# Kernel tuning notes

Hardware: AMD Instinct MI355X
Metric: run time of the kernel (lower is better)

The kernel has to match this reference:

```python
import jax, jax.numpy as jnp
import numpy as np

NUM_EXPERTS = 8
TOP_K = 2


def setup_inputs() -> dict:
    key = jax.random.key(0)
    k1, k2, k3, k4, k5 = jax.random.split(key, 5)
    B, S, H, F, E = 4, 1024, 1024, 2048, NUM_EXPERTS
    return {
        "hidden_states": jax.random.normal(k1, (B, S, H), dtype=jnp.float32),
        "gate_w": jax.random.normal(k2, (H, E), dtype=jnp.float32) * 0.02,
        "w1": jax.random.normal(k3, (E, H, F), dtype=jnp.float32) * 0.02,
        "w2": jax.random.normal(k4, (E, F, H), dtype=jnp.float32) * 0.02,
        "w3": jax.random.normal(k5, (E, H, F), dtype=jnp.float32) * 0.02,
    }


def reference(hidden_states, gate_w, w1, w2, w3):
    """Mixtral MoE block: router softmax -> top-2 -> SwiGLU expert FFN -> weighted combine.

    Same math as Gmm (sort + grouped GEMM + scatter): each token passes through its
    top-k experts' FFNs (silu(x@w1) * (x@w3)) @ w2, then the outputs are combined
    with the renormalized top-k routing weights.
    """
    B, S, H = hidden_states.shape
    E = w1.shape[0]
    x = hidden_states.reshape(-1, H)                       # [m, H]
    m = x.shape[0]

    router_logits = x @ gate_w                             # [m, E]
    probs = jax.nn.softmax(router_logits, axis=-1)
    top_w, top_i = jax.lax.top_k(probs, TOP_K)             # [m, k]
    top_w = top_w / jnp.sum(top_w, axis=-1, keepdims=True)

    # dense routing matrix [m, E] (top-k indices are distinct per row)
    route = jnp.zeros((m, E), dtype=x.dtype)
    route = route.at[jnp.arange(m)[:, None], top_i].set(top_w)

    out = jnp.zeros_like(x)
    for e in range(E):  # fixed small expert count; accumulate to keep memory low
        h = jax.nn.silu(x @ w1[e]) * (x @ w3[e])           # [m, F]
        out = out + route[:, e:e + 1] * (h @ w2[e])        # [m, H]

    return out.reshape(B, S, H)
```

## Files before the change

### kernel.cpp

```cpp
#include <hip/hip_runtime.h>

typedef __attribute__((ext_vector_type(8))) short bf16x8;
typedef __attribute__((ext_vector_type(4))) float f32x4;

#define MTOK 4096
#define HD 1024
#define FD 2048
#define NEXP 8
#define MAXT 72

struct Ctl {
  int counts[NEXP];
  int cursor[NEXP];
  int totalTiles;
  int _pad[7];
  int4 tileMap[MAXT];
  int topE[MTOK][2];
  float topW[MTOK][2];
  int pos[MTOK][2];
  int rowTok[2 * MTOK];
};

__device__ __forceinline__ unsigned short f2bf(float f) {
  unsigned int u = __float_as_uint(f);
  unsigned int r = u + 0x7fffu + ((u >> 16) & 1u);
  return (unsigned short)(r >> 16);
}
__device__ __forceinline__ float bf2f(unsigned short s) {
  return __uint_as_float(((unsigned int)s) << 16);
}
__device__ __forceinline__ unsigned int pk2(float a, float b) {
  return (unsigned int)f2bf(a) | ((unsigned int)f2bf(b) << 16);
}
__device__ __forceinline__ void gload16(const void* g, void* l) {
  __builtin_amdgcn_global_load_lds(
      (const __attribute__((address_space(1))) void*)g,
      (__attribute__((address_space(3))) void*)l, 16, 0, 0);
}

__global__ void k_tr(const float* __restrict__ in, unsigned short* __restrict__ outp,
                     int K, int N) {
  __shared__ float tile[64][65];
  int ntn = N >> 6, ntk = K >> 6;
  int bid = blockIdx.x;
  int e = bid / (ntk * ntn);
  int rem = bid % (ntk * ntn);
  int kt = rem / ntn, nt = rem % ntn;
  const float* src = in + (size_t)e * K * N + (size_t)(kt * 64) * N + nt * 64;
  unsigned short* dst = outp + (size_t)e * N * K + (size_t)(nt * 64) * K + kt * 64;
  int t = threadIdx.x;
  int nl = t & 63, kq = t >> 6;
#pragma unroll
  for (int i = 0; i < 16; i++) {
    int kl = kq * 16 + i;
    tile[kl][nl] = src[(size_t)kl * N + nl];
  }
  __syncthreads();
  int n2 = t >> 2, kc = (t & 3) * 16;
  unsigned int pk[8];
#pragma unroll
  for (int j = 0; j < 8; j++)
    pk[j] = pk2(tile[kc + 2 * j][n2], tile[kc + 2 * j + 1][n2]);
  *(uint4*)(dst + (size_t)n2 * K + kc) = make_uint4(pk[0], pk[1], pk[2], pk[3]);
  *(uint4*)(dst + (size_t)n2 * K + kc + 8) = make_uint4(pk[4], pk[5], pk[6], pk[7]);
}

__global__ void k_cvt_x(const float* __restrict__ x, unsigned short* __restrict__ xb) {
  int i = blockIdx.x * 256 + threadIdx.x;
  const float4* s = (const float4*)x;
  float4 a = s[i * 2], b = s[i * 2 + 1];
  *(uint4*)(xb + (size_t)i * 8) =
      make_uint4(pk2(a.x, a.y), pk2(a.z, a.w), pk2(b.x, b.y), pk2(b.z, b.w));
}

__global__ void k_router(const float* __restrict__ x, const float* __restrict__ gw,
                         Ctl* __restrict__ ctl) {
  int gt = blockIdx.x * 256 + threadIdx.x;
  int tok = gt >> 6;
  int lane = gt & 63;
  const float* xr = x + (size_t)tok * HD;
  float acc[NEXP] = {};
#pragma unroll
  for (int it = 0; it < 4; it++) {
    int h0 = it * 256 + lane * 4;
    float4 xv = *(const float4*)(xr + h0);
    float xs[4] = {xv.x, xv.y, xv.z, xv.w};
#pragma unroll
    for (int j = 0; j < 4; j++) {
      float4 g0 = *(const float4*)(gw + (size_t)(h0 + j) * 8);
      float4 g1 = *(const float4*)(gw + (size_t)(h0 + j) * 8 + 4);
      acc[0] += xs[j] * g0.x; acc[1] += xs[j] * g0.y;
      acc[2] += xs[j] * g0.z; acc[3] += xs[j] * g0.w;
      acc[4] += xs[j] * g1.x; acc[5] += xs[j] * g1.y;
      acc[6] += xs[j] * g1.z; acc[7] += xs[j] * g1.w;
    }
  }
#pragma unroll
  for (int off = 32; off > 0; off >>= 1) {
#pragma unroll
    for (int e = 0; e < NEXP; e++) acc[e] += __shfl_xor(acc[e], off);
  }
  if (lane == 0) {
    float l0 = -1e30f, l1 = -1e30f; int i0 = 0, i1 = 0;
#pragma unroll
    for (int e = 0; e < NEXP; e++) {
      float v = acc[e];
      if (v > l0) { l1 = l0; i1 = i0; l0 = v; i0 = e; }
      else if (v > l1) { l1 = v; i1 = e; }
    }
    float w0 = 1.f / (1.f + __expf(l1 - l0));
    ctl->topE[tok][0] = i0; ctl->topE[tok][1] = i1;
    ctl->topW[tok][0] = w0; ctl->topW[tok][1] = 1.f - w0;
  }
}

__global__ void k_count(Ctl* __restrict__ ctl) {
  __shared__ int lcnt[NEXP];
  int t = threadIdx.x;
  if (t < NEXP) lcnt[t] = 0;
  __syncthreads();
  int tok = blockIdx.x * 512 + t;
  atomicAdd(&lcnt[ctl->topE[tok][0]], 1);
  atomicAdd(&lcnt[ctl->topE[tok][1]], 1);
  __syncthreads();
  if (t < NEXP && lcnt[t]) atomicAdd(&ctl->counts[t], lcnt[t]);
}

__global__ void k_setup(Ctl* __restrict__ ctl) {
  if (threadIdx.x == 0 && blockIdx.x == 0) {
    int off = 0, t = 0;
    for (int e = 0; e < NEXP; e++) {
      ctl->cursor[e] = off;
      int c = ctl->counts[e];
      int nt = (c + 127) >> 7;
      for (int i = 0; i < nt; i++) {
        if (t < MAXT)
          ctl->tileMap[t] = make_int4(e, off + i * 128, min(128, c - i * 128), 0);
        t++;
      }
      off += c;
    }
    ctl->totalTiles = t;
    for (; t < MAXT; t++) ctl->tileMap[t] = make_int4(0, 0, 0, 0);
  }
}

__global__ void k_scatter(Ctl* __restrict__ ctl) {
  __shared__ int lcur[NEXP];
  __shared__ int gbase[NEXP];
  int t = threadIdx.x;
  int tok = blockIdx.x * 512 + t;
  if (t < NEXP) lcur[t] = 0;
  __syncthreads();
  int e0 = ctl->topE[tok][0];
  int e1 = ctl->topE[tok][1];
  int r0 = atomicAdd(&lcur[e0], 1);
  int r1 = atomicAdd(&lcur[e1], 1);
  __syncthreads();
  if (t < NEXP) gbase[t] = lcur[t] ? atomicAdd(&ctl->cursor[t], lcur[t]) : 0;
  __syncthreads();
  int p0 = gbase[e0] + r0;
  int p1 = gbase[e1] + r1;
  ctl->rowTok[p0] = tok; ctl->pos[tok][0] = p0;
  ctl->rowTok[p1] = tok; ctl->pos[tok][1] = p1;
}

__launch_bounds__(512, 2)
__global__ void k_gemm1(const unsigned short* __restrict__ xb,
                        const unsigned short* __restrict__ w1t,
                        const unsigned short* __restrict__ w3t,
                        unsigned short* __restrict__ hg,
                        const Ctl* __restrict__ ctl) {
  __shared__ __align__(1024) unsigned char lds[2][3][8192];
  int nwg = MAXT * (FD / 128);
  int bid = blockIdx.x;
  int swz = (bid & 7) * (nwg >> 3) + (bid >> 3);
  int rt = swz % MAXT, ct = swz / MAXT;
  int4 tm = ctl->tileMap[rt];
  if (tm.z == 0) return;
  int e = tm.x, grow0 = tm.y, nrows = tm.z;
  int t = threadIdx.x;

  int r = t >> 2;
  int cl = (t & 3) ^ ((r >> 1) & 3);
  int rA = min(r, nrows - 1);
  int tok = ctl->rowTok[grow0 + rA];
  const unsigned short* aG  = xb  + (size_t)tok * HD + cl * 8;
  const unsigned short* b1G = w1t + ((size_t)e * FD + ct * 128 + r) * HD + cl * 8;
  const unsigned short* b3G = w3t + ((size_t)e * FD + ct * 128 + r) * HD + cl * 8;
  unsigned char* ldsDstA  = &lds[0][0][t * 16];
  unsigned char* ldsDstB1 = &lds[0][1][t * 16];
  unsigned char* ldsDstB3 = &lds[0][2][t * 16];

  int lane = t & 63, wv = t >> 6, wr = wv >> 2, wc = wv & 3;
  int lm = lane & 15, lk = lane >> 4;
  int aOff[4], bOff[2];
#pragma unroll
  for (int ma = 0; ma < 4; ma++) {
    int row = wr * 64 + ma * 16 + lm;
    aOff[ma] = row * 64 + ((lk ^ ((row >> 1) & 3)) << 4);
  }
#pragma unroll
  for (int nb = 0; nb < 2; nb++) {
    int row = wc * 32 + nb * 16 + lm;
    bOff[nb] = row * 64 + ((lk ^ ((row >> 1) & 3)) << 4);
  }

  f32x4 accA[4][2] = {};
  f32x4 accC[4][2] = {};

  const int NK = HD / 32;
  gload16(aG, ldsDstA); gload16(b1G, ldsDstB1); gload16(b3G, ldsDstB3);
  for (int kt = 0; kt < NK; kt++) {
    int b = kt & 1;
    if (kt + 1 < NK) {
      size_t ko = (size_t)(kt + 1) * 32;
      int nbuf = b ^ 1;
      gload16(aG + ko,  ldsDstA  + nbuf * 3 * 8192);
      gload16(b1G + ko, ldsDstB1 + nbuf * 3 * 8192);
      gload16(b3G + ko, ldsDstB3 + nbuf * 3 * 8192);
      asm volatile("s_waitcnt vmcnt(3)" ::: "memory");
    } else {
      asm volatile("s_waitcnt vmcnt(0)" ::: "memory");
    }
    __builtin_amdgcn_s_barrier();
    asm volatile("" ::: "memory");
    const unsigned char* pA  = &lds[b][0][0];
    const unsigned char* pB1 = &lds[b][1][0];
    const unsigned char* pB3 = &lds[b][2][0];
    bf16x8 af[4], bf1[2], bf3[2];
#pragma unroll
    for (int ma = 0; ma < 4; ma++) af[ma] = *(const bf16x8*)(pA + aOff[ma]);
#pragma unroll
    for (int nb = 0; nb < 2; nb++) {
      bf1[nb] = *(const bf16x8*)(pB1 + bOff[nb]);
      bf3[nb] = *(const bf16x8*)(pB3 + bOff[nb]);
    }
#pragma unroll
    for (int nb = 0; nb < 2; nb++)
#pragma unroll
      for (int ma = 0; ma < 4; ma++) {
        accA[ma][nb] = __builtin_amdgcn_mfma_f32_16x16x32_bf16(af[ma], bf1[nb], accA[ma][nb], 0, 0, 0);
        accC[ma][nb] = __builtin_amdgcn_mfma_f32_16x16x32_bf16(af[ma], bf3[nb], accC[ma][nb], 0, 0, 0);
      }
    asm volatile("" ::: "memory");
    __builtin_amdgcn_s_barrier();
  }

#pragma unroll
  for (int ma = 0; ma < 4; ma++) {
    int lrowBase = wr * 64 + ma * 16 + lk * 4;
#pragma unroll
    for (int nb = 0; nb < 2; nb++) {
      int col = ct * 128 + wc * 32 + nb * 16 + lm;
#pragma unroll
      for (int rr = 0; rr < 4; rr++) {
        int lrow = lrowBase + rr;
        if (lrow < nrows) {
          float a = accA[ma][nb][rr];
          float c = accC[ma][nb][rr];
          float hv = a / (1.f + __expf(-a)) * c;
          hg[(size_t)(grow0 + lrow) * FD + col] = f2bf(hv);
        }
      }
    }
  }
}

__launch_bounds__(512, 2)
__global__ void k_gemm2(const unsigned short* __restrict__ hg,
                        const unsigned short* __restrict__ w2t,
                        unsigned short* __restrict__ og,
                        const Ctl* __restrict__ ctl) {
  __shared__ __align__(1024) unsigned char lds[2][2][8192];
  int nwg = MAXT * (HD / 128);
  int bid = blockIdx.x;
  int swz = (bid & 7) * (nwg >> 3) + (bid >> 3);
  int rt = swz % MAXT, ct = swz / MAXT;
  int4 tm = ctl->tileMap[rt];
  if (tm.z == 0) return;
  int e = tm.x, grow0 = tm.y, nrows = tm.z;
  int t = threadIdx.x;

  int r = t >> 2;
  int cl = (t & 3) ^ ((r >> 1) & 3);
  int rA = min(r, nrows - 1);
  const unsigned short* aG = hg  + (size_t)(grow0 + rA) * FD + cl * 8;
  const unsigned short* bG = w2t + ((size_t)e * HD + ct * 128 + r) * FD + cl * 8;
  unsigned char* ldsDstA = &lds[0][0][t * 16];
  unsigned char* ldsDstB = &lds[0][1][t * 16];

  int lane = t & 63, wv = t >> 6, wr = wv >> 2, wc = wv & 3;
  int lm = lane & 15, lk = lane >> 4;
  int aOff[4], bOff[2];
#pragma unroll
  for (int ma = 0; ma < 4; ma++) {
    int row = wr * 64 + ma * 16 + lm;
    aOff[ma] = row * 64 + ((lk ^ ((row >> 1) & 3)) << 4);
  }
#pragma unroll
  for (int nb = 0; nb < 2; nb++) {
    int row = wc * 32 + nb * 16 + lm;
    bOff[nb] = row * 64 + ((lk ^ ((row >> 1) & 3)) << 4);
  }

  f32x4 acc[4][2] = {};
  const int NK = FD / 32;
  gload16(aG, ldsDstA); gload16(bG, ldsDstB);
  for (int kt = 0; kt < NK; kt++) {
    int b = kt & 1;
    if (kt + 1 < NK) {
      size_t ko = (size_t)(kt + 1) * 32;
      int nbuf = b ^ 1;
      gload16(aG + ko, ldsDstA + nbuf * 2 * 8192);
      gload16(bG + ko, ldsDstB + nbuf * 2 * 8192);
      asm volatile("s_waitcnt vmcnt(2)" ::: "memory");
    } else {
      asm volatile("s_waitcnt vmcnt(0)" ::: "memory");
    }
    __builtin_amdgcn_s_barrier();
    asm volatile("" ::: "memory");
    const unsigned char* pA = &lds[b][0][0];
    const unsigned char* pB = &lds[b][1][0];
    bf16x8 af[4], bfr[2];
#pragma unroll
    for (int ma = 0; ma < 4; ma++) af[ma] = *(const bf16x8*)(pA + aOff[ma]);
#pragma unroll
    for (int nb = 0; nb < 2; nb++) bfr[nb] = *(const bf16x8*)(pB + bOff[nb]);
#pragma unroll
    for (int nb = 0; nb < 2; nb++)
#pragma unroll
      for (int ma = 0; ma < 4; ma++)
        acc[ma][nb] = __builtin_amdgcn_mfma_f32_16x16x32_bf16(af[ma], bfr[nb], acc[ma][nb], 0, 0, 0);
    asm volatile("" ::: "memory");
    __builtin_amdgcn_s_barrier();
  }

#pragma unroll
  for (int ma = 0; ma < 4; ma++) {
    int lrowBase = wr * 64 + ma * 16 + lk * 4;
#pragma unroll
    for (int nb = 0; nb < 2; nb++) {
      int col = ct * 128 + wc * 32 + nb * 16 + lm;
#pragma unroll
      for (int rr = 0; rr < 4; rr++) {
        int lrow = lrowBase + rr;
        if (lrow < nrows)
          og[(size_t)(grow0 + lrow) * HD + col] = f2bf(acc[ma][nb][rr]);
      }
    }
  }
}

__global__ void k_combine(const unsigned short* __restrict__ og, float* __restrict__ out,
                          const Ctl* __restrict__ ctl) {
  int tok = blockIdx.x;
  int tid = threadIdx.x;
  int p0 = ctl->pos[tok][0], p1 = ctl->pos[tok][1];
  float w0 = ctl->topW[tok][0], w1 = ctl->topW[tok][1];
  uint2 a = *(const uint2*)(og + (size_t)p0 * HD + tid * 4);
  uint2 b = *(const uint2*)(og + (size_t)p1 * HD + tid * 4);
  float4 o;
  o.x = w0 * bf2f((unsigned short)(a.x & 0xffffu)) + w1 * bf2f((unsigned short)(b.x & 0xffffu));
  o.y = w0 * bf2f((unsigned short)(a.x >> 16))     + w1 * bf2f((unsigned short)(b.x >> 16));
  o.z = w0 * bf2f((unsigned short)(a.y & 0xffffu)) + w1 * bf2f((unsigned short)(b.y & 0xffffu));
  o.w = w0 * bf2f((unsigned short)(a.y >> 16))     + w1 * bf2f((unsigned short)(b.y >> 16));
  *(float4*)(out + (size_t)tok * HD + tid * 4) = o;
}

extern "C" void kernel_launch(void* const* d_in, const int* in_sizes, int n_in,
                              void* d_out, int out_size, void* d_ws, size_t ws_size,
                              hipStream_t stream) {
  const float* x  = (const float*)d_in[0];
  const float* gw = (const float*)d_in[1];
  const float* w1 = (const float*)d_in[2];
  const float* w2 = (const float*)d_in[3];
  const float* w3 = (const float*)d_in[4];
  float* out = (float*)d_out;

  char* ws = (char*)d_ws;
  unsigned short* hg  = (unsigned short*)(ws);
  unsigned short* og  = (unsigned short*)(ws + (size_t)(32u << 20));
  unsigned short* xb  = (unsigned short*)(ws + (size_t)(48u << 20));
  unsigned short* wAt = (unsigned short*)(ws + (size_t)(56u << 20));
  unsigned short* wBt = (unsigned short*)(ws + (size_t)(88u << 20));
  Ctl* ctl = (Ctl*)(ws + (size_t)(120u << 20));

  hipMemsetAsync(ctl->counts, 0, sizeof(int) * NEXP, stream);
  k_tr<<<dim3(8 * 16 * 32), 256, 0, stream>>>(w1, wAt, HD, FD);
  k_tr<<<dim3(8 * 16 * 32), 256, 0, stream>>>(w3, wBt, HD, FD);
  k_cvt_x<<<dim3(2048), 256, 0, stream>>>(x, xb);
  k_router<<<dim3(MTOK / 4), 256, 0, stream>>>(x, gw, ctl);
  k_count<<<dim3(MTOK / 512), 512, 0, stream>>>(ctl);
  k_setup<<<1, 64, 0, stream>>>(ctl);
  k_scatter<<<dim3(MTOK / 512), 512, 0, stream>>>(ctl);
  k_gemm1<<<dim3(MAXT * (FD / 128)), 512, 0, stream>>>(xb, wAt, wBt, hg, ctl);
  k_tr<<<dim3(8 * 32 * 16), 256, 0, stream>>>(w2, wAt, FD, HD);
  k_gemm2<<<dim3(MAXT * (HD / 128)), 512, 0, stream>>>(hg, wAt, og, ctl);
  k_combine<<<dim3(MTOK), 256, 0, stream>>>(og, out, ctl);
}
```

Measured before the change: 400.6 us.

## Fuse prep kernels, vectorize transpose, parallelize setup, retile gemm2 to 128x64

Merges the w1/w3 transposes and the x conversion into one prep launch, and moves the counts memset into the router kernel. The transpose now does float4 loads into a padded tile. Tile-map setup is spread across 64 lanes instead of one thread. gemm2 moves from 512 threads with 128x128 tiles to 256 threads with 128x64 tiles, doubling the number of workgroups. This trades per-block B reuse for more parallelism, since gemm2 otherwise fills the GPU with few blocks.

```diff
diff --git a/kernel.cpp b/kernel.cpp
--- a/kernel.cpp
+++ b/kernel.cpp
@@ -38,22 +38,22 @@
       (__attribute__((address_space(3))) void*)l, 16, 0, 0);
 }
 
-__global__ void k_tr(const float* __restrict__ in, unsigned short* __restrict__ outp,
-                     int K, int N) {
-  __shared__ float tile[64][65];
+__device__ __forceinline__ void tr_body(const float* __restrict__ in,
+                                        unsigned short* __restrict__ outp,
+                                        int K, int N, int bid, float (*tile)[68]) {
   int ntn = N >> 6, ntk = K >> 6;
-  int bid = blockIdx.x;
   int e = bid / (ntk * ntn);
   int rem = bid % (ntk * ntn);
   int kt = rem / ntn, nt = rem % ntn;
   const float* src = in + (size_t)e * K * N + (size_t)(kt * 64) * N + nt * 64;
   unsigned short* dst = outp + (size_t)e * N * K + (size_t)(nt * 64) * K + kt * 64;
   int t = threadIdx.x;
-  int nl = t & 63, kq = t >> 6;
-#pragma unroll
-  for (int i = 0; i < 16; i++) {
-    int kl = kq * 16 + i;
-    tile[kl][nl] = src[(size_t)kl * N + nl];
+  int nl4 = t & 15, kr = t >> 4;
+#pragma unroll
+  for (int i = 0; i < 4; i++) {
+    int row = kr + i * 16;
+    float4 v = *(const float4*)(src + (size_t)row * N + nl4 * 4);
+    *(float4*)&tile[row][nl4 * 4] = v;
   }
   __syncthreads();
   int n2 = t >> 2, kc = (t & 3) * 16;
@@ -65,16 +65,34 @@
   *(uint4*)(dst + (size_t)n2 * K + kc + 8) = make_uint4(pk[4], pk[5], pk[6], pk[7]);
 }
 
-__global__ void k_cvt_x(const float* __restrict__ x, unsigned short* __restrict__ xb) {
-  int i = blockIdx.x * 256 + threadIdx.x;
-  const float4* s = (const float4*)x;
-  float4 a = s[i * 2], b = s[i * 2 + 1];
-  *(uint4*)(xb + (size_t)i * 8) =
-      make_uint4(pk2(a.x, a.y), pk2(a.z, a.w), pk2(b.x, b.y), pk2(b.z, b.w));
+__global__ void k_prep(const float* __restrict__ w1, const float* __restrict__ w3,
+                       const float* __restrict__ x,
+                       unsigned short* __restrict__ w1t, unsigned short* __restrict__ w3t,
+                       unsigned short* __restrict__ xb) {
+  __shared__ float tile[64][68];
+  int bid = blockIdx.x;
+  if (bid < 4096) {
+    tr_body(w1, w1t, HD, FD, bid, tile);
+  } else if (bid < 8192) {
+    tr_body(w3, w3t, HD, FD, bid - 4096, tile);
+  } else {
+    int i = (bid - 8192) * 256 + threadIdx.x;
+    const float4* s = (const float4*)x;
+    float4 a = s[i * 2], b = s[i * 2 + 1];
+    *(uint4*)(xb + (size_t)i * 8) =
+        make_uint4(pk2(a.x, a.y), pk2(a.z, a.w), pk2(b.x, b.y), pk2(b.z, b.w));
+  }
+}
+
+__global__ void k_tr(const float* __restrict__ in, unsigned short* __restrict__ outp,
+                     int K, int N) {
+  __shared__ float tile[64][68];
+  tr_body(in, outp, K, N, blockIdx.x, tile);
 }
 
 __global__ void k_router(const float* __restrict__ x, const float* __restrict__ gw,
                          Ctl* __restrict__ ctl) {
+  if (blockIdx.x == 0 && threadIdx.x < NEXP) ctl->counts[threadIdx.x] = 0;
   int gt = blockIdx.x * 256 + threadIdx.x;
   int tok = gt >> 6;
   int lane = gt & 63;
@@ -127,21 +145,27 @@
 }
 
 __global__ void k_setup(Ctl* __restrict__ ctl) {
-  if (threadIdx.x == 0 && blockIdx.x == 0) {
-    int off = 0, t = 0;
-    for (int e = 0; e < NEXP; e++) {
-      ctl->cursor[e] = off;
-      int c = ctl->counts[e];
-      int nt = (c + 127) >> 7;
-      for (int i = 0; i < nt; i++) {
-        if (t < MAXT)
-          ctl->tileMap[t] = make_int4(e, off + i * 128, min(128, c - i * 128), 0);
-        t++;
-      }
-      off += c;
-    }
-    ctl->totalTiles = t;
-    for (; t < MAXT; t++) ctl->tileMap[t] = make_int4(0, 0, 0, 0);
+  int lane = threadIdx.x;
+  int myC[NEXP], myOff[NEXP], myTb[NEXP];
+  int off = 0, t = 0;
+#pragma unroll
+  for (int e = 0; e < NEXP; e++) {
+    int c = ctl->counts[e];
+    myC[e] = c; myOff[e] = off; myTb[e] = t;
+    off += c; t += (c + 127) >> 7;
+  }
+  if (lane < NEXP) ctl->cursor[lane] = myOff[lane];
+  if (lane == 0) ctl->totalTiles = t;
+  for (int i = lane; i < MAXT; i += 64) {
+    int4 v = make_int4(0, 0, 0, 0);
+    if (i < t) {
+      int e = 0;
+#pragma unroll
+      for (int q = 1; q < NEXP; q++) if (myTb[q] <= i) e = q;
+      int j = i - myTb[e];
+      v = make_int4(e, myOff[e] + j * 128, min(128, myC[e] - j * 128), 0);
+    }
+    ctl->tileMap[i] = v;
   }
 }
 
@@ -267,13 +291,13 @@
   }
 }
 
-__launch_bounds__(512, 2)
+__launch_bounds__(256, 2)
 __global__ void k_gemm2(const unsigned short* __restrict__ hg,
                         const unsigned short* __restrict__ w2t,
                         unsigned short* __restrict__ og,
                         const Ctl* __restrict__ ctl) {
-  __shared__ __align__(1024) unsigned char lds[2][2][8192];
-  int nwg = MAXT * (HD / 128);
+  __shared__ __align__(1024) unsigned char lds[2][12288];
+  int nwg = MAXT * (HD / 64);
   int bid = blockIdx.x;
   int swz = (bid & 7) * (nwg >> 3) + (bid >> 3);
   int rt = swz % MAXT, ct = swz / MAXT;
@@ -282,15 +306,19 @@
   int e = tm.x, grow0 = tm.y, nrows = tm.z;
   int t = threadIdx.x;
 
-  int r = t >> 2;
-  int cl = (t & 3) ^ ((r >> 1) & 3);
-  int rA = min(r, nrows - 1);
-  const unsigned short* aG = hg  + (size_t)(grow0 + rA) * FD + cl * 8;
-  const unsigned short* bG = w2t + ((size_t)e * HD + ct * 128 + r) * FD + cl * 8;
-  unsigned char* ldsDstA = &lds[0][0][t * 16];
-  unsigned char* ldsDstB = &lds[0][1][t * 16];
-
-  int lane = t & 63, wv = t >> 6, wr = wv >> 2, wc = wv & 3;
+  int rA0 = t >> 2, rA1 = 64 + (t >> 2);
+  int cl0 = (t & 3) ^ ((rA0 >> 1) & 3);
+  int cl1 = (t & 3) ^ ((rA1 >> 1) & 3);
+  const unsigned short* aG0 = hg + (size_t)(grow0 + min(rA0, nrows - 1)) * FD + cl0 * 8;
+  const unsigned short* aG1 = hg + (size_t)(grow0 + min(rA1, nrows - 1)) * FD + cl1 * 8;
+  int rB = t >> 2;
+  int clB = (t & 3) ^ ((rB >> 1) & 3);
+  const unsigned short* bG = w2t + ((size_t)e * HD + ct * 64 + rB) * FD + clB * 8;
+  unsigned char* ldsA0 = &lds[0][t * 16];
+  unsigned char* ldsA1 = &lds[0][4096 + t * 16];
+  unsigned char* ldsB  = &lds[0][8192 + t * 16];
+
+  int lane = t & 63, wv = t >> 6, wr = wv >> 1, wc = wv & 1;
   int lm = lane & 15, lk = lane >> 4;
   int aOff[4], bOff[2];
 #pragma unroll
@@ -301,32 +329,32 @@
 #pragma unroll
   for (int nb = 0; nb < 2; nb++) {
     int row = wc * 32 + nb * 16 + lm;
-    bOff[nb] = row * 64 + ((lk ^ ((row >> 1) & 3)) << 4);
+    bOff[nb] = 8192 + row * 64 + ((lk ^ ((row >> 1) & 3)) << 4);
   }
 
   f32x4 acc[4][2] = {};
   const int NK = FD / 32;
-  gload16(aG, ldsDstA); gload16(bG, ldsDstB);
+  gload16(aG0, ldsA0); gload16(aG1, ldsA1); gload16(bG, ldsB);
   for (int kt = 0; kt < NK; kt++) {
     int b = kt & 1;
     if (kt + 1 < NK) {
       size_t ko = (size_t)(kt + 1) * 32;
       int nbuf = b ^ 1;
-      gload16(aG + ko, ldsDstA + nbuf * 2 * 8192);
-      gload16(bG + ko, ldsDstB + nbuf * 2 * 8192);
-      asm volatile("s_waitcnt vmcnt(2)" ::: "memory");
+      gload16(aG0 + ko, ldsA0 + nbuf * 12288);
+      gload16(aG1 + ko, ldsA1 + nbuf * 12288);
+      gload16(bG + ko,  ldsB  + nbuf * 12288);
+      asm volatile("s_waitcnt vmcnt(3)" ::: "memory");
     } else {
       asm volatile("s_waitcnt vmcnt(0)" ::: "memory");
     }
     __builtin_amdgcn_s_barrier();
     asm volatile("" ::: "memory");
-    const unsigned char* pA = &lds[b][0][0];
-    const unsigned char* pB = &lds[b][1][0];
+    const unsigned char* pL = &lds[b][0];
     bf16x8 af[4], bfr[2];
 #pragma unroll
-    for (int ma = 0; ma < 4; ma++) af[ma] = *(const bf16x8*)(pA + aOff[ma]);
-#pragma unroll
-    for (int nb = 0; nb < 2; nb++) bfr[nb] = *(const bf16x8*)(pB + bOff[nb]);
+    for (int ma = 0; ma < 4; ma++) af[ma] = *(const bf16x8*)(pL + aOff[ma]);
+#pragma unroll
+    for (int nb = 0; nb < 2; nb++) bfr[nb] = *(const bf16x8*)(pL + bOff[nb]);
 #pragma unroll
     for (int nb = 0; nb < 2; nb++)
 #pragma unroll
@@ -341,7 +369,7 @@
     int lrowBase = wr * 64 + ma * 16 + lk * 4;
 #pragma unroll
     for (int nb = 0; nb < 2; nb++) {
-      int col = ct * 128 + wc * 32 + nb * 16 + lm;
+      int col = ct * 64 + wc * 32 + nb * 16 + lm;
 #pragma unroll
       for (int rr = 0; rr < 4; rr++) {
         int lrow = lrowBase + rr;
@@ -386,16 +414,13 @@
   unsigned short* wBt = (unsigned short*)(ws + (size_t)(88u << 20));
   Ctl* ctl = (Ctl*)(ws + (size_t)(120u << 20));
 
-  hipMemsetAsync(ctl->counts, 0, sizeof(int) * NEXP, stream);
-  k_tr<<<dim3(8 * 16 * 32), 256, 0, stream>>>(w1, wAt, HD, FD);
-  k_tr<<<dim3(8 * 16 * 32), 256, 0, stream>>>(w3, wBt, HD, FD);
-  k_cvt_x<<<dim3(2048), 256, 0, stream>>>(x, xb);
+  k_prep<<<dim3(8192 + 2048), 256, 0, stream>>>(w1, w3, x, wAt, wBt, xb);
   k_router<<<dim3(MTOK / 4), 256, 0, stream>>>(x, gw, ctl);
   k_count<<<dim3(MTOK / 512), 512, 0, stream>>>(ctl);
   k_setup<<<1, 64, 0, stream>>>(ctl);
   k_scatter<<<dim3(MTOK / 512), 512, 0, stream>>>(ctl);
   k_gemm1<<<dim3(MAXT * (FD / 128)), 512, 0, stream>>>(xb, wAt, wBt, hg, ctl);
   k_tr<<<dim3(8 * 32 * 16), 256, 0, stream>>>(w2, wAt, FD, HD);
-  k_gemm2<<<dim3(MAXT * (HD / 128)), 512, 0, stream>>>(hg, wAt, og, ctl);
+  k_gemm2<<<dim3(MAXT * (HD / 64)), 256, 0, stream>>>(hg, wAt, og, ctl);
   k_combine<<<dim3(MTOK), 256, 0, stream>>>(og, out, ctl);
 }
```

Result: slower. 421.9 us (+5.3%).
